# Kernel optimization log

Hardware: AMD Instinct MI355X
Metric: run time of the kernel (lower is better)

## Reference

```python
import jax, jax.numpy as jnp
import numpy as np

B, S, D, H = 128, 64, 512, 256  # batch, seq_len, model_dim, lstm hidden (=D//2)
VOCAB, SEL, MLPD, CLS = 32000, 128, 1024, 3


def setup_inputs() -> dict:
    key = jax.random.key(0)
    ks = jax.random.split(key, 10)
    sc = 0.02
    return {
        "sentences": jax.random.randint(ks[0], (B, S), 0, VOCAB),
        "transitions": jnp.zeros((B, 2 * S - 1), dtype=jnp.int32),  # unused by pyramid path
        "embed_table": jax.random.normal(ks[1], (VOCAB, D), jnp.float32) * sc,
        "comp_W": jax.random.normal(ks[2], (2 * H, 5 * H), jnp.float32) * sc,
        "comp_b": jnp.zeros((5 * H,), jnp.float32),
        "sel_W1": jax.random.normal(ks[3], (2 * D, SEL), jnp.float32) * sc,
        "sel_b1": jnp.zeros((SEL,), jnp.float32),
        "sel_W2": jax.random.normal(ks[4], (SEL, 1), jnp.float32) * sc,
        "sel_b2": jnp.zeros((1,), jnp.float32),
        "mlp_W0": jax.random.normal(ks[5], (D, MLPD), jnp.float32) * sc,
        "mlp_b0": jnp.zeros((MLPD,), jnp.float32),
        "mlp_W1": jax.random.normal(ks[6], (MLPD, MLPD), jnp.float32) * sc,
        "mlp_b1": jnp.zeros((MLPD,), jnp.float32),
        "mlp_Wout": jax.random.normal(ks[7], (MLPD, CLS), jnp.float32) * sc,
        "mlp_bout": jnp.zeros((CLS,), jnp.float32),
    }


def _tree_lstm(left, right, W, b):
    # left/right: [..., D] state vectors holding [h; c]
    h_l, c_l = left[..., :H], left[..., H:]
    h_r, c_r = right[..., :H], right[..., H:]
    gates = jnp.concatenate([h_l, h_r], axis=-1) @ W + b  # [..., 5H]
    i, fl, fr, u, o = jnp.split(gates, 5, axis=-1)
    c = (jax.nn.sigmoid(fl) * c_l + jax.nn.sigmoid(fr) * c_r
         + jax.nn.sigmoid(i) * jnp.tanh(u))
    h = jax.nn.sigmoid(o) * jnp.tanh(c)
    return jnp.concatenate([h, c], axis=-1)


def reference(sentences, transitions, embed_table, comp_W, comp_b,
              sel_W1, sel_b1, sel_W2, sel_b2,
              mlp_W0, mlp_b0, mlp_W1, mlp_b1, mlp_Wout, mlp_bout):
    # embed (context encoder = identity)
    states = embed_table[sentences]  # [B, S, D]
    # soft pyramid: seq_len-1 merge layers, each shrinking the row by 1
    for layer in range(S - 1, 0, -1):
        left = states[:, :-1]   # [B, layer, D]
        right = states[:, 1:]   # [B, layer, D]
        comp = _tree_lstm(left, right, comp_W, comp_b)  # [B, layer, D]
        sel_in = jnp.concatenate([left, right], axis=-1)  # [B, layer, 2D]
        hid = jnp.tanh(sel_in @ sel_W1 + sel_b1)
        logits = (hid @ sel_W2 + sel_b2)[..., 0]  # [B, layer]
        probs = jax.nn.softmax(logits, axis=1)
        cs = jnp.cumsum(probs, axis=1)
        copy_right = (cs - probs)[..., None]          # sum probs[:p]
        copy_left = (cs[:, -1:] - cs)[..., None]      # sum probs[p+1:]
        select = probs[..., None]
        states = copy_left * left + copy_right * right + select * comp
    h = states[:, 0]  # [B, D]
    # 2-layer MLP classifier (eval mode: no dropout, no LN)
    h1 = jax.nn.relu(h @ mlp_W0 + mlp_b0)
    h2 = jax.nn.relu(h1 @ mlp_W1 + mlp_b1)
    return h2 @ mlp_Wout + mlp_bout  # [B, CLS]
```

## Files before the change

### kernel.cpp

```cpp
#include <hip/hip_runtime.h>
#include <hip/hip_bf16.h>
#include <math.h>

#define B_ 128
#define S_ 64
#define D_ 512
#define H_ 256
#define SEL_ 128
#define MLPD_ 1024
#define CLS_ 3

typedef __attribute__((ext_vector_type(8))) short bf16x8;
typedef __attribute__((ext_vector_type(4))) float f32x4;

__device__ __forceinline__ float sigf(float x) { return 1.f / (1.f + expf(-x)); }

__device__ __forceinline__ ushort bf16r(float x) {
    uint u = __float_as_uint(x);
    return (ushort)((u + 0x7fffu + ((u >> 16) & 1u)) >> 16);
}
__device__ __forceinline__ float bf2f(ushort h) { return __uint_as_float(((uint)h) << 16); }

__device__ __forceinline__ int xcd_chunk(int bid, int nb) {
    int q = nb >> 3, r = nb & 7;
    int xcd = bid & 7, j = bid >> 3;
    return (xcd < r ? xcd * (q + 1) : r * (q + 1) + (xcd - r) * q) + j;
}

__global__ __launch_bounds__(256) void k_embed(const int* __restrict__ sent,
                                               const float* __restrict__ emb,
                                               ushort* __restrict__ oh,
                                               ushort* __restrict__ ol) {
    int idx = blockIdx.x * 256 + threadIdx.x;
    int row = idx >> 7;
    int k4 = (idx & 127) << 2;
    int tok = sent[row];
    float4 v = *(const float4*)(emb + (size_t)tok * D_ + k4);
    ushort4 h, l;
    h.x = bf16r(v.x); l.x = bf16r(v.x - bf2f(h.x));
    h.y = bf16r(v.y); l.y = bf16r(v.y - bf2f(h.y));
    h.z = bf16r(v.z); l.z = bf16r(v.z - bf2f(h.z));
    h.w = bf16r(v.w); l.w = bf16r(v.w - bf2f(h.w));
    *(ushort4*)(oh + (size_t)row * D_ + k4) = h;
    *(ushort4*)(ol + (size_t)row * D_ + k4) = l;
}

__global__ __launch_bounds__(256) void k_tsplit(const float* __restrict__ src,
                                                ushort* __restrict__ dh,
                                                ushort* __restrict__ dl,
                                                int K, int N) {
    __shared__ float t[64][65];
    int n0 = blockIdx.x * 64, k0 = blockIdx.y * 64;
    int tx = threadIdx.x & 63, ty = threadIdx.x >> 6;
    for (int i = ty; i < 64; i += 4)
        t[i][tx] = src[(size_t)(k0 + i) * N + n0 + tx];
    __syncthreads();
    for (int i = ty; i < 64; i += 4) {
        float v = t[tx][i];
        ushort h = bf16r(v);
        size_t o = (size_t)(n0 + i) * K + k0 + tx;
        dh[o] = h;
        dl[o] = bf16r(v - bf2f(h));
    }
}

__global__ __launch_bounds__(256) void k_sellogit(const ushort* __restrict__ sh,
                                                  const ushort* __restrict__ sl,
                                                  const ushort* __restrict__ w1h,
                                                  const ushort* __restrict__ w1l,
                                                  const float* __restrict__ b1,
                                                  const float* __restrict__ W2,
                                                  const float* __restrict__ b2,
                                                  float* __restrict__ logits,
                                                  int N, int M, int cdiv) {
    __shared__ __align__(16) ushort sAm[2][64][40];
    __shared__ __align__(16) ushort sBm[2][128][40];
    __shared__ int rb[64];
    __shared__ float lpart[2][64];
    int w = xcd_chunk(blockIdx.x, gridDim.x);
    int r0 = w * 64;
    int tid = threadIdx.x, l = tid & 63, wid = tid >> 6;
    int wm = wid >> 1, wn = wid & 1;
    int lr = l & 15, lk = (l >> 4) << 3;

    if (tid < 64) {
        int g = r0 + tid;
        int q = (int)(((long long)g * cdiv) >> 20);
        rb[tid] = (g + q) * 512;
    }
    __syncthreads();

    float bias[4], w2v[4];
#pragma unroll
    for (int tj = 0; tj < 4; tj++) {
        int c = wn * 64 + tj * 16 + lr;
        bias[tj] = b1[c];
        w2v[tj] = W2[c];
    }

    const ushort* aSrc[2]; ushort* aDst[2];
#pragma unroll
    for (int i = 0; i < 2; i++) {
        int idx = tid + i * 256;
        int p = idx >> 8, rem = idx & 255;
        int r = rem >> 2, s = rem & 3;
        aSrc[i] = (p ? sl : sh) + rb[r] + s * 8;
        aDst[i] = &sAm[p][r][s * 8];
    }
    const ushort* bSrc[4]; ushort* bDst[4];
#pragma unroll
    for (int j = 0; j < 4; j++) {
        int idx = tid + j * 256;
        int p = (idx >= 512) ? 1 : 0;
        int rem = idx - p * 512;
        int br = rem >> 2, s = rem & 3;
        bSrc[j] = (p ? w1l : w1h) + br * 1024 + s * 8;
        bDst[j] = &sBm[p][br][s * 8];
    }

    f32x4 z = {0.f, 0.f, 0.f, 0.f};
    f32x4 acc[2][4] = {{z, z, z, z}, {z, z, z, z}};
    bf16x8 gA[2], gB[4];

#define SSTAGE_LOAD(kk) do {                                               \
        _Pragma("unroll")                                                  \
        for (int i = 0; i < 2; i++) gA[i] = *(const bf16x8*)(aSrc[i] + (kk)); \
        _Pragma("unroll")                                                  \
        for (int j = 0; j < 4; j++) gB[j] = *(const bf16x8*)(bSrc[j] + (kk)); \
    } while (0)
#define SSTAGE_WRITE() do {                                                \
        _Pragma("unroll")                                                  \
        for (int i = 0; i < 2; i++) *(bf16x8*)aDst[i] = gA[i];             \
        _Pragma("unroll")                                                  \
        for (int j = 0; j < 4; j++) *(bf16x8*)bDst[j] = gB[j];             \
    } while (0)

    SSTAGE_LOAD(0);
    SSTAGE_WRITE();
    __syncthreads();

    for (int ks = 0; ks < 32; ks++) {
        if (ks < 31) SSTAGE_LOAD((ks + 1) * 32);
        bf16x8 fa[2][2], fb[2][4];
#pragma unroll
        for (int t = 0; t < 2; t++) {
            int ar = wm * 32 + t * 16 + lr;
            fa[0][t] = *(const bf16x8*)&sAm[0][ar][lk];
            fa[1][t] = *(const bf16x8*)&sAm[1][ar][lk];
        }
#pragma unroll
        for (int tj = 0; tj < 4; tj++) {
            int bc = wn * 64 + tj * 16 + lr;
            fb[0][tj] = *(const bf16x8*)&sBm[0][bc][lk];
            fb[1][tj] = *(const bf16x8*)&sBm[1][bc][lk];
        }
#pragma unroll
        for (int ti = 0; ti < 2; ti++)
#pragma unroll
            for (int tj = 0; tj < 4; tj++) {
                acc[ti][tj] = __builtin_amdgcn_mfma_f32_16x16x32_bf16(fa[0][ti], fb[0][tj], acc[ti][tj], 0, 0, 0);
                acc[ti][tj] = __builtin_amdgcn_mfma_f32_16x16x32_bf16(fa[0][ti], fb[1][tj], acc[ti][tj], 0, 0, 0);
                acc[ti][tj] = __builtin_amdgcn_mfma_f32_16x16x32_bf16(fa[1][ti], fb[0][tj], acc[ti][tj], 0, 0, 0);
            }
        __syncthreads();
        if (ks < 31) {
            SSTAGE_WRITE();
            __syncthreads();
        }
    }
#undef SSTAGE_LOAD
#undef SSTAGE_WRITE

    float part[2][4];
#pragma unroll
    for (int ti = 0; ti < 2; ti++)
#pragma unroll
        for (int r = 0; r < 4; r++) {
            float s = 0.f;
#pragma unroll
            for (int tj = 0; tj < 4; tj++)
                s += tanhf(acc[ti][tj][r] + bias[tj]) * w2v[tj];
            part[ti][r] = s;
        }
#pragma unroll
    for (int off = 1; off < 16; off <<= 1)
#pragma unroll
        for (int ti = 0; ti < 2; ti++)
#pragma unroll
            for (int r = 0; r < 4; r++)
                part[ti][r] += __shfl_xor(part[ti][r], off);
    if ((l & 15) == 0) {
#pragma unroll
        for (int ti = 0; ti < 2; ti++)
#pragma unroll
            for (int r = 0; r < 4; r++)
                lpart[wn][wm * 32 + ti * 16 + ((l >> 4) << 2) + r] = part[ti][r];
    }
    __syncthreads();
    if (tid < 64) {
        int g = r0 + tid;
        logits[g] = lpart[0][tid] + lpart[1][tid] + b2[0];
    }
}

__global__ __launch_bounds__(256) void k_compose(const ushort* __restrict__ sh,
                                                 const ushort* __restrict__ sl,
                                                 const ushort* __restrict__ wth,
                                                 const ushort* __restrict__ wtl,
                                                 const float* __restrict__ cbias,
                                                 const float* __restrict__ logits,
                                                 ushort* __restrict__ dh,
                                                 ushort* __restrict__ dl,
                                                 float* __restrict__ root,
                                                 int N, int M, int cdiv) {
    __shared__ __align__(16) ushort sAm[2][64][40];
    __shared__ __align__(16) ushort sBm[2][160][40];
    __shared__ int rb[64];
    __shared__ float slog[192];
    __shared__ float scoef[64][3];
    int w = xcd_chunk(blockIdx.x, gridDim.x);
    int cx = w & 7, ry = w >> 3;
    int tid = threadIdx.x, l = tid & 63, wid = tid >> 6;
    int wm = wid >> 1, wn = wid & 1;
    int r0 = ry * 64;
    int cb_blk = cx * 32;
    int cbw = cb_blk + wn * 16;
    int lr = l & 15, lk = (l >> 4) << 3;

    int blo = (int)(((long long)r0 * cdiv) >> 20);
    int bhi = (int)(((long long)(r0 + 63) * cdiv) >> 20);
    int cnt = (bhi - blo + 1) * N;
    if (tid < 64) {
        int g = r0 + tid;
        int q = (int)(((long long)g * cdiv) >> 20);
        rb[tid] = (g + q) * 512;
    }
    if (tid < cnt) slog[tid] = logits[blo * N + tid];
    __syncthreads();

    if (tid < 64) {
        int g = r0 + tid;
        int b = (int)(((long long)g * cdiv) >> 20);
        int j = g - b * N;
        int o = (b - blo) * N;
        float mx = -1e30f;
        for (int k = 0; k < N; k++) mx = fmaxf(mx, slog[o + k]);
        float tot = 0.f, cs = 0.f, pj = 0.f;
        for (int k = 0; k < N; k++) {
            float e = expf(slog[o + k] - mx);
            tot += e;
            if (k <= j) cs += e;
            if (k == j) pj = e;
        }
        float inv = 1.f / tot;
        scoef[tid][0] = (tot - cs) * inv;
        scoef[tid][1] = (cs - pj) * inv;
        scoef[tid][2] = pj * inv;
    }

    float bias[5];
#pragma unroll
    for (int gt = 0; gt < 5; gt++) bias[gt] = cbias[gt * 256 + cbw + lr];

    const ushort* aSrc[2]; ushort* aDst[2];
#pragma unroll
    for (int i = 0; i < 2; i++) {
        int idx = tid + i * 256;
        int p = idx >> 8, rem = idx & 255;
        int r = rem >> 2, s = rem & 3;
        aSrc[i] = (p ? sl : sh) + rb[r] + s * 8;
        aDst[i] = &sAm[p][r][s * 8];
    }
    const ushort* bSrc[5]; ushort* bDst[5];
#pragma unroll
    for (int j = 0; j < 5; j++) {
        int idx = tid + j * 256;
        int p = (idx >= 640) ? 1 : 0;
        int rem = idx - p * 640;
        int br = rem >> 2, s = rem & 3;
        int col = (br >> 5) * 256 + cb_blk + (br & 31);
        bSrc[j] = (p ? wtl : wth) + col * 512 + s * 8;
        bDst[j] = &sBm[p][br][s * 8];
    }

    f32x4 z = {0.f, 0.f, 0.f, 0.f};
    f32x4 acc[2][5] = {{z, z, z, z, z}, {z, z, z, z, z}};
    bf16x8 gA[2], gB[5];

#define CSTAGE_LOAD(kk) do {                                               \
        int koff_ = ((kk) < 256) ? (kk) : (kk) + 256;                      \
        _Pragma("unroll")                                                  \
        for (int i = 0; i < 2; i++) gA[i] = *(const bf16x8*)(aSrc[i] + koff_); \
        _Pragma("unroll")                                                  \
        for (int j = 0; j < 5; j++) gB[j] = *(const bf16x8*)(bSrc[j] + (kk)); \
    } while (0)
#define CSTAGE_WRITE() do {                                                \
        _Pragma("unroll")                                                  \
        for (int i = 0; i < 2; i++) *(bf16x8*)aDst[i] = gA[i];             \
        _Pragma("unroll")                                                  \
        for (int j = 0; j < 5; j++) *(bf16x8*)bDst[j] = gB[j];             \
    } while (0)

    CSTAGE_LOAD(0);
    CSTAGE_WRITE();
    __syncthreads();

    for (int ks = 0; ks < 16; ks++) {
        if (ks < 15) CSTAGE_LOAD((ks + 1) * 32);
        bf16x8 fa[2][2], fb[2][5];
#pragma unroll
        for (int t = 0; t < 2; t++) {
            int ar = wm * 32 + t * 16 + lr;
            fa[0][t] = *(const bf16x8*)&sAm[0][ar][lk];
            fa[1][t] = *(const bf16x8*)&sAm[1][ar][lk];
        }
#pragma unroll
        for (int gt = 0; gt < 5; gt++) {
            int br = gt * 32 + wn * 16 + lr;
            fb[0][gt] = *(const bf16x8*)&sBm[0][br][lk];
            fb[1][gt] = *(const bf16x8*)&sBm[1][br][lk];
        }
#pragma unroll
        for (int gt = 0; gt < 5; gt++)
#pragma unroll
            for (int t = 0; t < 2; t++) {
                acc[t][gt] = __builtin_amdgcn_mfma_f32_16x16x32_bf16(fa[0][t], fb[0][gt], acc[t][gt], 0, 0, 0);
                acc[t][gt] = __builtin_amdgcn_mfma_f32_16x16x32_bf16(fa[0][t], fb[1][gt], acc[t][gt], 0, 0, 0);
                acc[t][gt] = __builtin_amdgcn_mfma_f32_16x16x32_bf16(fa[1][t], fb[0][gt], acc[t][gt], 0, 0, 0);
            }
        __syncthreads();
        if (ks < 15) {
            CSTAGE_WRITE();
            __syncthreads();
        }
    }
#undef CSTAGE_LOAD
#undef CSTAGE_WRITE

#pragma unroll
    for (int t = 0; t < 2; t++)
#pragma unroll
        for (int r = 0; r < 4; r++) {
            int lrow = wm * 32 + t * 16 + ((l >> 4) << 2) + r;
            int m = r0 + lrow;
            size_t sb = (size_t)rb[lrow];
            int c = cbw + lr;
            float cl = scoef[lrow][0], cr = scoef[lrow][1], sel = scoef[lrow][2];
            float h_l = bf2f(sh[sb + c])       + bf2f(sl[sb + c]);
            float c_l = bf2f(sh[sb + 256 + c]) + bf2f(sl[sb + 256 + c]);
            float h_r = bf2f(sh[sb + 512 + c]) + bf2f(sl[sb + 512 + c]);
            float c_r = bf2f(sh[sb + 768 + c]) + bf2f(sl[sb + 768 + c]);
            float gi  = acc[t][0][r] + bias[0];
            float gfl = acc[t][1][r] + bias[1];
            float gfr = acc[t][2][r] + bias[2];
            float gu  = acc[t][3][r] + bias[3];
            float go  = acc[t][4][r] + bias[4];
            float cn = sigf(gfl) * c_l + sigf(gfr) * c_r + sigf(gi) * tanhf(gu);
            float hn = sigf(go) * tanhf(cn);
            float oh = cl * h_l + cr * h_r + sel * hn;
            float oc = cl * c_l + cr * c_r + sel * cn;
            size_t ob = (size_t)m * 512 + c;
            ushort hh = bf16r(oh);
            dh[ob] = hh;
            dl[ob] = bf16r(oh - bf2f(hh));
            ushort hc = bf16r(oc);
            dh[ob + 256] = hc;
            dl[ob + 256] = bf16r(oc - bf2f(hc));
            if (N == 1) {
                root[ob] = oh;
                root[ob + 256] = oc;
            }
        }
}

template <int ACT>
__global__ __launch_bounds__(256) void k_gemm(const float* __restrict__ A,
                                              const float* __restrict__ W,
                                              const float* __restrict__ bias,
                                              float* __restrict__ C,
                                              int M, int K, int Nc) {
    __shared__ float Xs[32][36];
    __shared__ float Ws[32][64];
    int tid = threadIdx.x;
    int r0 = blockIdx.x * 32, c0 = blockIdx.y * 64;
    int ct = tid & 15, rt = tid >> 4;
    float acc[2][4];
#pragma unroll
    for (int r = 0; r < 2; r++)
#pragma unroll
        for (int q = 0; q < 4; q++) {
            int c = c0 + ct * 4 + q;
            acc[r][q] = (c < Nc) ? bias[c] : 0.f;
        }
    for (int kk = 0; kk < K; kk += 32) {
        __syncthreads();
        {
            int m = tid >> 3, k4 = (tid & 7) << 2;
            float4 v = {0.f, 0.f, 0.f, 0.f};
            if (r0 + m < M) v = *(const float4*)(A + (size_t)(r0 + m) * K + kk + k4);
            Xs[k4 + 0][m] = v.x; Xs[k4 + 1][m] = v.y; Xs[k4 + 2][m] = v.z; Xs[k4 + 3][m] = v.w;
        }
#pragma unroll
        for (int i = 0; i < 2; i++) {
            int idx = tid + i * 256;
            int k = idx >> 4, c4 = (idx & 15) << 2;
            int c = c0 + c4;
            float4 v = {0.f, 0.f, 0.f, 0.f};
            if (c + 3 < Nc) {
                v = *(const float4*)(W + (size_t)(kk + k) * Nc + c);
            } else {
                float tmp[4] = {0.f, 0.f, 0.f, 0.f};
                for (int j = 0; j < 4; j++)
                    if (c + j < Nc) tmp[j] = W[(size_t)(kk + k) * Nc + c + j];
                v = *(float4*)tmp;
            }
            *(float4*)&Ws[k][c4] = v;
        }
        __syncthreads();
#pragma unroll
        for (int k = 0; k < 32; k++) {
            float x0 = Xs[k][rt * 2], x1 = Xs[k][rt * 2 + 1];
            float wv[4];
            *(float4*)wv = *(const float4*)&Ws[k][ct * 4];
#pragma unroll
            for (int q = 0; q < 4; q++) { acc[0][q] += x0 * wv[q]; acc[1][q] += x1 * wv[q]; }
        }
    }
#pragma unroll
    for (int r = 0; r < 2; r++) {
        int g = r0 + rt * 2 + r;
        if (g >= M) continue;
#pragma unroll
        for (int q = 0; q < 4; q++) {
            int c = c0 + ct * 4 + q;
            if (c >= Nc) continue;
            float v = acc[r][q];
            if (ACT == 1) v = fmaxf(v, 0.f);
            C[(size_t)g * Nc + c] = v;
        }
    }
}

extern "C" void kernel_launch(void* const* d_in, const int* in_sizes, int n_in,
                              void* d_out, int out_size, void* d_ws, size_t ws_size,
                              hipStream_t stream) {
    const int*   sent     = (const int*)d_in[0];
    const float* emb      = (const float*)d_in[2];
    const float* comp_W   = (const float*)d_in[3];
    const float* comp_b   = (const float*)d_in[4];
    const float* sel_W1   = (const float*)d_in[5];
    const float* sel_b1   = (const float*)d_in[6];
    const float* sel_W2   = (const float*)d_in[7];
    const float* sel_b2   = (const float*)d_in[8];
    const float* mlp_W0   = (const float*)d_in[9];
    const float* mlp_b0   = (const float*)d_in[10];
    const float* mlp_W1   = (const float*)d_in[11];
    const float* mlp_b1   = (const float*)d_in[12];
    const float* mlp_Wout = (const float*)d_in[13];
    const float* mlp_bout = (const float*)d_in[14];
    float* outp = (float*)d_out;

    char* p = (char*)d_ws;
    ushort* sh0  = (ushort*)p; p += (size_t)B_ * S_ * D_ * 2;
    ushort* sl0  = (ushort*)p; p += (size_t)B_ * S_ * D_ * 2;
    ushort* sh1  = (ushort*)p; p += (size_t)B_ * S_ * D_ * 2;
    ushort* sl1  = (ushort*)p; p += (size_t)B_ * S_ * D_ * 2;
    ushort* wth  = (ushort*)p; p += (size_t)1280 * 512 * 2;
    ushort* wtl  = (ushort*)p; p += (size_t)1280 * 512 * 2;
    ushort* w1th = (ushort*)p; p += (size_t)128 * 1024 * 2;
    ushort* w1tl = (ushort*)p; p += (size_t)128 * 1024 * 2;
    float*  logits = (float*)p; p += (size_t)B_ * 63 * 4;
    float*  root = (float*)p;  p += (size_t)B_ * D_ * 4;
    float*  h1   = (float*)p;  p += (size_t)B_ * MLPD_ * 4;
    float*  h2   = (float*)p;  p += (size_t)B_ * MLPD_ * 4;

    k_embed<<<dim3(4096), dim3(256), 0, stream>>>(sent, emb, sh0, sl0);
    k_tsplit<<<dim3(20, 8), dim3(256), 0, stream>>>(comp_W, wth, wtl, 512, 1280);
    k_tsplit<<<dim3(2, 16), dim3(256), 0, stream>>>(sel_W1, w1th, w1tl, 1024, 128);

    ushort* shs = sh0; ushort* sls = sl0;
    ushort* shd = sh1; ushort* sld = sl1;
    for (int L = S_; L >= 2; --L) {
        int N = L - 1;
        int M = B_ * N;
        int cdiv = (1048576 + N - 1) / N;
        k_sellogit<<<dim3(M / 64), dim3(256), 0, stream>>>(shs, sls, w1th, w1tl, sel_b1,
                                                           sel_W2, sel_b2, logits, N, M, cdiv);
        k_compose<<<dim3(8 * (M / 64)), dim3(256), 0, stream>>>(shs, sls, wth, wtl, comp_b, logits,
                                                                shd, sld, root, N, M, cdiv);
        ushort* th = shs; shs = shd; shd = th;
        ushort* tl = sls; sls = sld; sld = tl;
    }

    k_gemm<1><<<dim3(4, 16), dim3(256), 0, stream>>>(root, mlp_W0, mlp_b0, h1, B_, 512, MLPD_);
    k_gemm<1><<<dim3(4, 16), dim3(256), 0, stream>>>(h1, mlp_W1, mlp_b1, h2, B_, 1024, MLPD_);
    k_gemm<0><<<dim3(4, 1), dim3(256), 0, stream>>>(h2, mlp_Wout, mlp_bout, outp, B_, 1024, CLS_);
}
```

Baseline: 4.145 ms.

## Move MLP head to split-bf16 MFMA kernels and halve sellogit row tile

The scalar fp32 MLP GEMMs are replaced by a split-bf16 (hi/lo) MFMA GEMM kernel. The root state is written in hi/lo bf16 form and the MLP weights are pre-split on the device. The 3-class output gets a small dedicated warp-reduction kernel. The selection-logit kernel's row tile shrinks from 64 to 32, doubling its grid to improve occupancy on the per-layer launches. In exchange there are extra weight-split launches and a small precision change from the three-term bf16 emulation in the MLP.

```diff
diff --git a/kernel.cpp b/kernel.cpp
--- a/kernel.cpp
+++ b/kernel.cpp
@@ -73,17 +73,17 @@
                                                   const float* __restrict__ b2,
                                                   float* __restrict__ logits,
                                                   int N, int M, int cdiv) {
-    __shared__ __align__(16) ushort sAm[2][64][40];
+    __shared__ __align__(16) ushort sAm[2][32][40];
     __shared__ __align__(16) ushort sBm[2][128][40];
-    __shared__ int rb[64];
-    __shared__ float lpart[2][64];
+    __shared__ int rb[32];
+    __shared__ float lpart[2][32];
     int w = xcd_chunk(blockIdx.x, gridDim.x);
-    int r0 = w * 64;
+    int r0 = w * 32;
     int tid = threadIdx.x, l = tid & 63, wid = tid >> 6;
-    int wm = wid >> 1, wn = wid & 1;
+    int rt2 = wid & 1, ch = wid >> 1;
     int lr = l & 15, lk = (l >> 4) << 3;
 
-    if (tid < 64) {
+    if (tid < 32) {
         int g = r0 + tid;
         int q = (int)(((long long)g * cdiv) >> 20);
         rb[tid] = (g + q) * 512;
@@ -93,20 +93,15 @@
     float bias[4], w2v[4];
 #pragma unroll
     for (int tj = 0; tj < 4; tj++) {
-        int c = wn * 64 + tj * 16 + lr;
+        int c = ch * 64 + tj * 16 + lr;
         bias[tj] = b1[c];
         w2v[tj] = W2[c];
     }
 
-    const ushort* aSrc[2]; ushort* aDst[2];
-#pragma unroll
-    for (int i = 0; i < 2; i++) {
-        int idx = tid + i * 256;
-        int p = idx >> 8, rem = idx & 255;
-        int r = rem >> 2, s = rem & 3;
-        aSrc[i] = (p ? sl : sh) + rb[r] + s * 8;
-        aDst[i] = &sAm[p][r][s * 8];
-    }
+    int pA = tid >> 7, remA = tid & 127;
+    int rA = remA >> 2, sA = remA & 3;
+    const ushort* aSrc = (pA ? sl : sh) + rb[rA] + sA * 8;
+    ushort* aDst = &sAm[pA][rA][sA * 8];
     const ushort* bSrc[4]; ushort* bDst[4];
 #pragma unroll
     for (int j = 0; j < 4; j++) {
@@ -119,18 +114,16 @@
     }
 
     f32x4 z = {0.f, 0.f, 0.f, 0.f};
-    f32x4 acc[2][4] = {{z, z, z, z}, {z, z, z, z}};
-    bf16x8 gA[2], gB[4];
+    f32x4 acc[4] = {z, z, z, z};
+    bf16x8 gA, gB[4];
 
 #define SSTAGE_LOAD(kk) do {                                               \
-        _Pragma("unroll")                                                  \
-        for (int i = 0; i < 2; i++) gA[i] = *(const bf16x8*)(aSrc[i] + (kk)); \
+        gA = *(const bf16x8*)(aSrc + (kk));                                \
         _Pragma("unroll")                                                  \
         for (int j = 0; j < 4; j++) gB[j] = *(const bf16x8*)(bSrc[j] + (kk)); \
     } while (0)
 #define SSTAGE_WRITE() do {                                                \
-        _Pragma("unroll")                                                  \
-        for (int i = 0; i < 2; i++) *(bf16x8*)aDst[i] = gA[i];             \
+        *(bf16x8*)aDst = gA;                                               \
         _Pragma("unroll")                                                  \
         for (int j = 0; j < 4; j++) *(bf16x8*)bDst[j] = gB[j];             \
     } while (0)
@@ -141,27 +134,24 @@
 
     for (int ks = 0; ks < 32; ks++) {
         if (ks < 31) SSTAGE_LOAD((ks + 1) * 32);
-        bf16x8 fa[2][2], fb[2][4];
-#pragma unroll
-        for (int t = 0; t < 2; t++) {
-            int ar = wm * 32 + t * 16 + lr;
-            fa[0][t] = *(const bf16x8*)&sAm[0][ar][lk];
-            fa[1][t] = *(const bf16x8*)&sAm[1][ar][lk];
+        bf16x8 fa[2], fb[2][4];
+        {
+            int ar = rt2 * 16 + lr;
+            fa[0] = *(const bf16x8*)&sAm[0][ar][lk];
+            fa[1] = *(const bf16x8*)&sAm[1][ar][lk];
         }
 #pragma unroll
         for (int tj = 0; tj < 4; tj++) {
-            int bc = wn * 64 + tj * 16 + lr;
+            int bc = ch * 64 + tj * 16 + lr;
             fb[0][tj] = *(const bf16x8*)&sBm[0][bc][lk];
             fb[1][tj] = *(const bf16x8*)&sBm[1][bc][lk];
         }
 #pragma unroll
-        for (int ti = 0; ti < 2; ti++)
-#pragma unroll
-            for (int tj = 0; tj < 4; tj++) {
-                acc[ti][tj] = __builtin_amdgcn_mfma_f32_16x16x32_bf16(fa[0][ti], fb[0][tj], acc[ti][tj], 0, 0, 0);
-                acc[ti][tj] = __builtin_amdgcn_mfma_f32_16x16x32_bf16(fa[0][ti], fb[1][tj], acc[ti][tj], 0, 0, 0);
-                acc[ti][tj] = __builtin_amdgcn_mfma_f32_16x16x32_bf16(fa[1][ti], fb[0][tj], acc[ti][tj], 0, 0, 0);
-            }
+        for (int tj = 0; tj < 4; tj++) {
+            acc[tj] = __builtin_amdgcn_mfma_f32_16x16x32_bf16(fa[0], fb[0][tj], acc[tj], 0, 0, 0);
+            acc[tj] = __builtin_amdgcn_mfma_f32_16x16x32_bf16(fa[0], fb[1][tj], acc[tj], 0, 0, 0);
+            acc[tj] = __builtin_amdgcn_mfma_f32_16x16x32_bf16(fa[1], fb[0][tj], acc[tj], 0, 0, 0);
+        }
         __syncthreads();
         if (ks < 31) {
             SSTAGE_WRITE();
@@ -171,36 +161,28 @@
 #undef SSTAGE_LOAD
 #undef SSTAGE_WRITE
 
-    float part[2][4];
-#pragma unroll
-    for (int ti = 0; ti < 2; ti++)
-#pragma unroll
-        for (int r = 0; r < 4; r++) {
-            float s = 0.f;
-#pragma unroll
-            for (int tj = 0; tj < 4; tj++)
-                s += tanhf(acc[ti][tj][r] + bias[tj]) * w2v[tj];
-            part[ti][r] = s;
-        }
+    float part[4];
+#pragma unroll
+    for (int r = 0; r < 4; r++) {
+        float s = 0.f;
+#pragma unroll
+        for (int tj = 0; tj < 4; tj++)
+            s += tanhf(acc[tj][r] + bias[tj]) * w2v[tj];
+        part[r] = s;
+    }
 #pragma unroll
     for (int off = 1; off < 16; off <<= 1)
 #pragma unroll
-        for (int ti = 0; ti < 2; ti++)
-#pragma unroll
-            for (int r = 0; r < 4; r++)
-                part[ti][r] += __shfl_xor(part[ti][r], off);
+        for (int r = 0; r < 4; r++)
+            part[r] += __shfl_xor(part[r], off);
     if ((l & 15) == 0) {
 #pragma unroll
-        for (int ti = 0; ti < 2; ti++)
-#pragma unroll
-            for (int r = 0; r < 4; r++)
-                lpart[wn][wm * 32 + ti * 16 + ((l >> 4) << 2) + r] = part[ti][r];
-    }
-    __syncthreads();
-    if (tid < 64) {
-        int g = r0 + tid;
-        logits[g] = lpart[0][tid] + lpart[1][tid] + b2[0];
-    }
+        for (int r = 0; r < 4; r++)
+            lpart[ch][rt2 * 16 + ((l >> 4) << 2) + r] = part[r];
+    }
+    __syncthreads();
+    if (tid < 32)
+        logits[r0 + tid] = lpart[0][tid] + lpart[1][tid] + b2[0];
 }
 
 __global__ __launch_bounds__(256) void k_compose(const ushort* __restrict__ sh,
@@ -211,7 +193,8 @@
                                                  const float* __restrict__ logits,
                                                  ushort* __restrict__ dh,
                                                  ushort* __restrict__ dl,
-                                                 float* __restrict__ root,
+                                                 ushort* __restrict__ rh,
+                                                 ushort* __restrict__ rl,
                                                  int N, int M, int cdiv) {
     __shared__ __align__(16) ushort sAm[2][64][40];
     __shared__ __align__(16) ushort sBm[2][160][40];
@@ -361,83 +344,143 @@
             float oc = cl * c_l + cr * c_r + sel * cn;
             size_t ob = (size_t)m * 512 + c;
             ushort hh = bf16r(oh);
-            dh[ob] = hh;
-            dl[ob] = bf16r(oh - bf2f(hh));
+            ushort hl = bf16r(oh - bf2f(hh));
             ushort hc = bf16r(oc);
-            dh[ob + 256] = hc;
-            dl[ob + 256] = bf16r(oc - bf2f(hc));
+            ushort lc = bf16r(oc - bf2f(hc));
+            dh[ob] = hh;       dl[ob] = hl;
+            dh[ob + 256] = hc; dl[ob + 256] = lc;
             if (N == 1) {
-                root[ob] = oh;
-                root[ob + 256] = oc;
+                rh[ob] = hh;       rl[ob] = hl;
+                rh[ob + 256] = hc; rl[ob + 256] = lc;
             }
         }
 }
 
-template <int ACT>
-__global__ __launch_bounds__(256) void k_gemm(const float* __restrict__ A,
-                                              const float* __restrict__ W,
-                                              const float* __restrict__ bias,
-                                              float* __restrict__ C,
-                                              int M, int K, int Nc) {
-    __shared__ float Xs[32][36];
-    __shared__ float Ws[32][64];
-    int tid = threadIdx.x;
-    int r0 = blockIdx.x * 32, c0 = blockIdx.y * 64;
-    int ct = tid & 15, rt = tid >> 4;
-    float acc[2][4];
-#pragma unroll
-    for (int r = 0; r < 2; r++)
-#pragma unroll
-        for (int q = 0; q < 4; q++) {
-            int c = c0 + ct * 4 + q;
-            acc[r][q] = (c < Nc) ? bias[c] : 0.f;
-        }
-    for (int kk = 0; kk < K; kk += 32) {
+template <int ACT, int SPLITOUT>
+__global__ __launch_bounds__(256) void k_mlp(const ushort* __restrict__ Ah,
+                                             const ushort* __restrict__ Al,
+                                             const ushort* __restrict__ Bh,
+                                             const ushort* __restrict__ Bl,
+                                             const float* __restrict__ bias,
+                                             ushort* __restrict__ oh,
+                                             ushort* __restrict__ ol,
+                                             float* __restrict__ of,
+                                             int K, int Nc) {
+    __shared__ __align__(16) ushort sAm[2][32][40];
+    __shared__ __align__(16) ushort sBm[2][128][40];
+    int r0 = blockIdx.x * 32, cb = blockIdx.y * 128;
+    int tid = threadIdx.x, l = tid & 63, wid = tid >> 6;
+    int rt2 = wid & 1, ch = wid >> 1;
+    int lr = l & 15, lk = (l >> 4) << 3;
+
+    float bias4[4];
+#pragma unroll
+    for (int tj = 0; tj < 4; tj++) bias4[tj] = bias[cb + ch * 64 + tj * 16 + lr];
+
+    int pA = tid >> 7, remA = tid & 127;
+    int rA = remA >> 2, sA = remA & 3;
+    const ushort* aSrc = (pA ? Al : Ah) + (size_t)(r0 + rA) * K + sA * 8;
+    ushort* aDst = &sAm[pA][rA][sA * 8];
+    const ushort* bSrc[4]; ushort* bDst[4];
+#pragma unroll
+    for (int j = 0; j < 4; j++) {
+        int idx = tid + j * 256;
+        int p = (idx >= 512) ? 1 : 0;
+        int rem = idx - p * 512;
+        int br = rem >> 2, s = rem & 3;
+        bSrc[j] = (p ? Bl : Bh) + (size_t)(cb + br) * K + s * 8;
+        bDst[j] = &sBm[p][br][s * 8];
+    }
+
+    f32x4 z = {0.f, 0.f, 0.f, 0.f};
+    f32x4 acc[4] = {z, z, z, z};
+    bf16x8 gA, gB[4];
+
+#define MSTAGE_LOAD(kk) do {                                               \
+        gA = *(const bf16x8*)(aSrc + (kk));                                \
+        _Pragma("unroll")                                                  \
+        for (int j = 0; j < 4; j++) gB[j] = *(const bf16x8*)(bSrc[j] + (kk)); \
+    } while (0)
+#define MSTAGE_WRITE() do {                                                \
+        *(bf16x8*)aDst = gA;                                               \
+        _Pragma("unroll")                                                  \
+        for (int j = 0; j < 4; j++) *(bf16x8*)bDst[j] = gB[j];             \
+    } while (0)
+
+    MSTAGE_LOAD(0);
+    MSTAGE_WRITE();
+    __syncthreads();
+
+    int nks = K >> 5;
+    for (int ks = 0; ks < nks; ks++) {
+        if (ks < nks - 1) MSTAGE_LOAD((ks + 1) * 32);
+        bf16x8 fa[2], fb[2][4];
+        {
+            int ar = rt2 * 16 + lr;
+            fa[0] = *(const bf16x8*)&sAm[0][ar][lk];
+            fa[1] = *(const bf16x8*)&sAm[1][ar][lk];
+        }
+#pragma unroll
+        for (int tj = 0; tj < 4; tj++) {
+            int bc = ch * 64 + tj * 16 + lr;
+            fb[0][tj] = *(const bf16x8*)&sBm[0][bc][lk];
+            fb[1][tj] = *(const bf16x8*)&sBm[1][bc][lk];
+        }
+#pragma unroll
+        for (int tj = 0; tj < 4; tj++) {
+            acc[tj] = __builtin_amdgcn_mfma_f32_16x16x32_bf16(fa[0], fb[0][tj], acc[tj], 0, 0, 0);
+            acc[tj] = __builtin_amdgcn_mfma_f32_16x16x32_bf16(fa[0], fb[1][tj], acc[tj], 0, 0, 0);
+            acc[tj] = __builtin_amdgcn_mfma_f32_16x16x32_bf16(fa[1], fb[0][tj], acc[tj], 0, 0, 0);
+        }
         __syncthreads();
-        {
-            int m = tid >> 3, k4 = (tid & 7) << 2;
-            float4 v = {0.f, 0.f, 0.f, 0.f};
-            if (r0 + m < M) v = *(const float4*)(A + (size_t)(r0 + m) * K + kk + k4);
-            Xs[k4 + 0][m] = v.x; Xs[k4 + 1][m] = v.y; Xs[k4 + 2][m] = v.z; Xs[k4 + 3][m] = v.w;
-        }
-#pragma unroll
-        for (int i = 0; i < 2; i++) {
-            int idx = tid + i * 256;
-            int k = idx >> 4, c4 = (idx & 15) << 2;
-            int c = c0 + c4;
-            float4 v = {0.f, 0.f, 0.f, 0.f};
-            if (c + 3 < Nc) {
-                v = *(const float4*)(W + (size_t)(kk + k) * Nc + c);
+        if (ks < nks - 1) {
+            MSTAGE_WRITE();
+            __syncthreads();
+        }
+    }
+#undef MSTAGE_LOAD
+#undef MSTAGE_WRITE
+
+#pragma unroll
+    for (int tj = 0; tj < 4; tj++)
+#pragma unroll
+        for (int r = 0; r < 4; r++) {
+            int grow = r0 + rt2 * 16 + ((l >> 4) << 2) + r;
+            int gcol = cb + ch * 64 + tj * 16 + lr;
+            float v = acc[tj][r] + bias4[tj];
+            if (ACT == 1) v = fmaxf(v, 0.f);
+            if (SPLITOUT) {
+                ushort h = bf16r(v);
+                oh[(size_t)grow * Nc + gcol] = h;
+                ol[(size_t)grow * Nc + gcol] = bf16r(v - bf2f(h));
             } else {
-                float tmp[4] = {0.f, 0.f, 0.f, 0.f};
-                for (int j = 0; j < 4; j++)
-                    if (c + j < Nc) tmp[j] = W[(size_t)(kk + k) * Nc + c + j];
-                v = *(float4*)tmp;
+                of[(size_t)grow * Nc + gcol] = v;
             }
-            *(float4*)&Ws[k][c4] = v;
-        }
-        __syncthreads();
-#pragma unroll
-        for (int k = 0; k < 32; k++) {
-            float x0 = Xs[k][rt * 2], x1 = Xs[k][rt * 2 + 1];
-            float wv[4];
-            *(float4*)wv = *(const float4*)&Ws[k][ct * 4];
-#pragma unroll
-            for (int q = 0; q < 4; q++) { acc[0][q] += x0 * wv[q]; acc[1][q] += x1 * wv[q]; }
-        }
-    }
-#pragma unroll
-    for (int r = 0; r < 2; r++) {
-        int g = r0 + rt * 2 + r;
-        if (g >= M) continue;
-#pragma unroll
-        for (int q = 0; q < 4; q++) {
-            int c = c0 + ct * 4 + q;
-            if (c >= Nc) continue;
-            float v = acc[r][q];
-            if (ACT == 1) v = fmaxf(v, 0.f);
-            C[(size_t)g * Nc + c] = v;
-        }
+        }
+}
+
+__global__ __launch_bounds__(64) void k_cls(const float* __restrict__ h2,
+                                            const float* __restrict__ Wout,
+                                            const float* __restrict__ bout,
+                                            float* __restrict__ out) {
+    int row = blockIdx.x, lane = threadIdx.x;
+    float s0 = 0.f, s1 = 0.f, s2 = 0.f;
+    for (int k = lane; k < 1024; k += 64) {
+        float v = h2[(size_t)row * 1024 + k];
+        s0 += v * Wout[k * 3 + 0];
+        s1 += v * Wout[k * 3 + 1];
+        s2 += v * Wout[k * 3 + 2];
+    }
+#pragma unroll
+    for (int o = 32; o >= 1; o >>= 1) {
+        s0 += __shfl_down(s0, o);
+        s1 += __shfl_down(s1, o);
+        s2 += __shfl_down(s2, o);
+    }
+    if (lane == 0) {
+        out[row * 3 + 0] = s0 + bout[0];
+        out[row * 3 + 1] = s1 + bout[1];
+        out[row * 3 + 2] = s2 + bout[2];
     }
 }
 
@@ -469,14 +512,22 @@
     ushort* wtl  = (ushort*)p; p += (size_t)1280 * 512 * 2;
     ushort* w1th = (ushort*)p; p += (size_t)128 * 1024 * 2;
     ushort* w1tl = (ushort*)p; p += (size_t)128 * 1024 * 2;
+    ushort* w0th = (ushort*)p; p += (size_t)1024 * 512 * 2;
+    ushort* w0tl = (ushort*)p; p += (size_t)1024 * 512 * 2;
+    ushort* w1mh = (ushort*)p; p += (size_t)1024 * 1024 * 2;
+    ushort* w1ml = (ushort*)p; p += (size_t)1024 * 1024 * 2;
     float*  logits = (float*)p; p += (size_t)B_ * 63 * 4;
-    float*  root = (float*)p;  p += (size_t)B_ * D_ * 4;
-    float*  h1   = (float*)p;  p += (size_t)B_ * MLPD_ * 4;
+    ushort* rh   = (ushort*)p; p += (size_t)B_ * D_ * 2;
+    ushort* rl   = (ushort*)p; p += (size_t)B_ * D_ * 2;
+    ushort* h1h  = (ushort*)p; p += (size_t)B_ * MLPD_ * 2;
+    ushort* h1l  = (ushort*)p; p += (size_t)B_ * MLPD_ * 2;
     float*  h2   = (float*)p;  p += (size_t)B_ * MLPD_ * 4;
 
     k_embed<<<dim3(4096), dim3(256), 0, stream>>>(sent, emb, sh0, sl0);
     k_tsplit<<<dim3(20, 8), dim3(256), 0, stream>>>(comp_W, wth, wtl, 512, 1280);
     k_tsplit<<<dim3(2, 16), dim3(256), 0, stream>>>(sel_W1, w1th, w1tl, 1024, 128);
+    k_tsplit<<<dim3(16, 8), dim3(256), 0, stream>>>(mlp_W0, w0th, w0tl, 512, 1024);
+    k_tsplit<<<dim3(16, 16), dim3(256), 0, stream>>>(mlp_W1, w1mh, w1ml, 1024, 1024);
 
     ushort* shs = sh0; ushort* sls = sl0;
     ushort* shd = sh1; ushort* sld = sl1;
@@ -484,15 +535,17 @@
         int N = L - 1;
         int M = B_ * N;
         int cdiv = (1048576 + N - 1) / N;
-        k_sellogit<<<dim3(M / 64), dim3(256), 0, stream>>>(shs, sls, w1th, w1tl, sel_b1,
+        k_sellogit<<<dim3(M / 32), dim3(256), 0, stream>>>(shs, sls, w1th, w1tl, sel_b1,
                                                            sel_W2, sel_b2, logits, N, M, cdiv);
         k_compose<<<dim3(8 * (M / 64)), dim3(256), 0, stream>>>(shs, sls, wth, wtl, comp_b, logits,
-                                                                shd, sld, root, N, M, cdiv);
+                                                                shd, sld, rh, rl, N, M, cdiv);
         ushort* th = shs; shs = shd; shd = th;
         ushort* tl = sls; sls = sld; sld = tl;
     }
 
-    k_gemm<1><<<dim3(4, 16), dim3(256), 0, stream>>>(root, mlp_W0, mlp_b0, h1, B_, 512, MLPD_);
-    k_gemm<1><<<dim3(4, 16), dim3(256), 0, stream>>>(h1, mlp_W1, mlp_b1, h2, B_, 1024, MLPD_);
-    k_gemm<0><<<dim3(4, 1), dim3(256), 0, stream>>>(h2, mlp_Wout, mlp_bout, outp, B_, 1024, CLS_);
-}
+    k_mlp<1, 1><<<dim3(4, 8), dim3(256), 0, stream>>>(rh, rl, w0th, w0tl, mlp_b0,
+                                                      h1h, h1l, nullptr, 512, MLPD_);
+    k_mlp<1, 0><<<dim3(4, 8), dim3(256), 0, stream>>>(h1h, h1l, w1mh, w1ml, mlp_b1,
+                                                      nullptr, nullptr, h2, 1024, MLPD_);
+    k_cls<<<dim3(B_), dim3(64), 0, stream>>>(h2, mlp_Wout, mlp_bout, outp);
+}
```

Result: faster. 3.691 ms (-10.9%).
